# Kernel optimization log

Hardware: AMD Instinct MI355X
Metric: run time of the kernel (lower is better)

The kernel has to match this reference:

```python
import jax, jax.numpy as jnp
import numpy as np

L, D, V, F4 = 12, 768, 50304, 3072
B, T = 4, 1024


def setup_inputs() -> dict:
    key = jax.random.key(0)
    ks = jax.random.split(key, 12)
    s = 0.02
    return {
        "idx": jax.random.randint(ks[0], (B, T), 0, V),
        "targets": jax.random.randint(ks[1], (B, T), 0, V),
        "wte": jax.random.normal(ks[2], (V, D), jnp.float32) * s,  # tied with lm_head
        "pos_embed": jax.random.normal(ks[3], (L, D), jnp.float32),  # per-block (1,1,D) learned pos embed
        "dyt_alpha": jnp.full((L, 3), 0.5, jnp.float32),  # dyt, dyt2, dyt3 alphas
        "dyt_w": jnp.ones((L, 3, D), jnp.float32),
        "dyt_b": jnp.zeros((L, 3, D), jnp.float32),
        "Wq": jax.random.normal(ks[4], (L, D, D), jnp.float32) * s,
        "Wk": jax.random.normal(ks[5], (L, D, D), jnp.float32) * s,
        "Wv": jax.random.normal(ks[6], (L, D, D), jnp.float32) * s,
        "Wp": jax.random.normal(ks[7], (L, D, D), jnp.float32) * s,
        "bp": jnp.zeros((L, D), jnp.float32),
        "We": jax.random.normal(ks[8], (L, F4, D), jnp.float32) * s,
        "be": jnp.zeros((L, F4), jnp.float32),
        "Wc": jax.random.normal(ks[9], (L, D, F4), jnp.float32) * s,
        "bc": jnp.zeros((L, D), jnp.float32),
    }


def _dyt(x, a, w, b):
    return jnp.tanh(a * x) * w + b


def _forward(idx, targets, wte, pos_embed, dyt_alpha, dyt_w, dyt_b,
             Wq, Wk, Wv, Wp, bp, We, be, Wc, bc):
    b, t = idx.shape
    x = wte[idx]  # (b,t,D)
    pos = jnp.arange(t)
    pbias = -jnp.abs(pos[None, :] - pos[:, None]).astype(x.dtype)  # (t,t) ALiBi-style bias
    scale = 1.0 / np.sqrt(D)  # note: source scales by sqrt(emb_dim), not head dim
    total_kl = jnp.asarray(0.0, x.dtype)
    for l in range(L):
        xl = x + pos_embed[l][None, None, :]
        prior = _dyt(xl, dyt_alpha[l, 2], dyt_w[l, 2], dyt_b[l, 2])  # dyt3
        h = _dyt(xl, dyt_alpha[l, 0], dyt_w[l, 0], dyt_b[l, 0])      # dyt (dropout=0)
        Q = jnp.einsum('btd,od->bto', h, Wq[l])
        K = jnp.einsum('btd,od->bto', h, Wk[l])
        Vv = jnp.einsum('btd,od->bto', h, Wv[l])
        scores = jnp.einsum('btd,bsd->bts', Q, K) * scale + pbias  # (b,t,t), no causal mask
        aw = jax.nn.softmax(scores, axis=-1)
        ao = jnp.einsum('bts,bsd->btd', aw, Vv)
        ao = jnp.einsum('btd,od->bto', ao, Wp[l]) + bp[l]
        h2 = _dyt(ao, dyt_alpha[l, 1], dyt_w[l, 1], dyt_b[l, 1])     # dyt2
        h2 = jax.nn.gelu(jnp.einsum('btd,fd->btf', h2, We[l]) + be[l], approximate=False)
        h2 = jnp.einsum('btf,df->btd', h2, Wc[l]) + bc[l]
        posterior = h2 + prior
        m = 0.5 * (prior + posterior)
        lm = jax.nn.log_softmax(m, axis=-1)
        mp = jnp.exp(lm)
        lp = jax.nn.log_softmax(prior, axis=-1)
        lq = jax.nn.log_softmax(posterior, axis=-1)
        # F.kl_div(log_p, q, reduction='batchmean') = sum(q*(log q - log_p)) / batch
        kl = 0.5 * (jnp.sum(mp * (lm - lp)) + jnp.sum(mp * (lm - lq))) / b
        total_kl = total_kl + kl
        x = posterior
    logits = jnp.einsum('btd,vd->btv', x[:, -1:, :], wte)  # (b,1,V)
    full_logits = jnp.einsum('btd,vd->btv', x, wte)
    lsm = jax.nn.log_softmax(full_logits, axis=-1)
    nll = -jnp.take_along_axis(lsm, targets[..., None], axis=-1).squeeze(-1)
    loss = jnp.mean(nll) + total_kl * 0.1
    return logits, loss


def reference(idx, targets, wte, pos_embed, dyt_alpha, dyt_w, dyt_b,
              Wq, Wk, Wv, Wp, bp, We, be, Wc, bc):
    return _forward(idx, targets, wte, pos_embed, dyt_alpha, dyt_w, dyt_b,
                    Wq, Wk, Wv, Wp, bp, We, be, Wc, bc)
```

## Files before the change

kernel.cpp:

```cpp
#include <hip/hip_runtime.h>
#include <hip/hip_bf16.h>

typedef __attribute__((ext_vector_type(8))) short bf16x8;
typedef __attribute__((ext_vector_type(4))) float f32x4;

__device__ __forceinline__ short f2bf(float f) {
  unsigned u = __float_as_uint(f);
  u = u + 0x7fffu + ((u >> 16) & 1u);
  return (short)(u >> 16);
}
__device__ __forceinline__ float bf2f(short s) {
  return __uint_as_float(((unsigned)(unsigned short)s) << 16);
}

#define GLOB_CAST(p) ((const __attribute__((address_space(1))) void*)(p))
#define LDS_CAST(p) ((__attribute__((address_space(3))) void*)(p))
#define GLL16(g, l) __builtin_amdgcn_global_load_lds(GLOB_CAST(g), LDS_CAST(l), 16, 0, 0)

constexpr int EP_BF16 = 0, EP_SCORES = 1, EP_DYT = 2, EP_GELU = 3, EP_PRIOR = 4, EP_QKVT = 5;

__global__ __launch_bounds__(256) void cvt_k(const float* __restrict__ src,
                                             short* __restrict__ dst, long n4) {
  const long s = (long)blockIdx.x * 256 + threadIdx.x;
  if (s >= n4) return;
  float4 v = ((const float4*)src)[s];
  short4 o = {f2bf(v.x), f2bf(v.y), f2bf(v.z), f2bf(v.w)};
  ((short4*)dst)[s] = o;
}

__global__ __launch_bounds__(256) void cvt_layer_k(
    const float* __restrict__ wq, const float* __restrict__ wk,
    const float* __restrict__ wv, const float* __restrict__ wp,
    const float* __restrict__ we, const float* __restrict__ wc,
    short* __restrict__ dst) {
  const long s = (long)blockIdx.x * 256 + threadIdx.x;
  const long e = s * 4;
  const float* src; long off;
  if (e < 589824)        { src = wq; off = e; }
  else if (e < 1179648)  { src = wk; off = e - 589824; }
  else if (e < 1769472)  { src = wv; off = e - 1179648; }
  else if (e < 2359296)  { src = wp; off = e - 1769472; }
  else if (e < 4718592)  { src = we; off = e - 2359296; }
  else                   { src = wc; off = e - 4718592; }
  float4 v = *(const float4*)(src + off);
  short4 o = {f2bf(v.x), f2bf(v.y), f2bf(v.z), f2bf(v.w)};
  *(short4*)(dst + e) = o;
}

__global__ __launch_bounds__(256) void cvt_all_k(
    const float* __restrict__ wq, const float* __restrict__ wk,
    const float* __restrict__ wv, const float* __restrict__ wp,
    const float* __restrict__ we, const float* __restrict__ wc,
    short* __restrict__ dst) {
  const long s = (long)blockIdx.x * 256 + threadIdx.x;
  if (s >= 21233664L) return;
  const long l = s / 1769472;
  const long e = (s - l * 1769472) * 4;
  const float* src; long off;
  if (e < 589824)        { src = wq + l * 589824;  off = e; }
  else if (e < 1179648)  { src = wk + l * 589824;  off = e - 589824; }
  else if (e < 1769472)  { src = wv + l * 589824;  off = e - 1179648; }
  else if (e < 2359296)  { src = wp + l * 589824;  off = e - 1769472; }
  else if (e < 4718592)  { src = we + l * 2359296; off = e - 2359296; }
  else                   { src = wc + l * 2359296; off = e - 4718592; }
  float4 v = *(const float4*)(src + off);
  short4 o = {f2bf(v.x), f2bf(v.y), f2bf(v.z), f2bf(v.w)};
  *(short4*)(dst + l * 7077888 + e) = o;
}

__global__ __launch_bounds__(256) void embed_head_k(
    const int* __restrict__ idx, const float* __restrict__ wte,
    const float* __restrict__ pos, const float* __restrict__ alp,
    const float* __restrict__ w, const float* __restrict__ b,
    float* __restrict__ x, float* __restrict__ prior, short* __restrict__ h) {
  const long s = (long)blockIdx.x * 256 + threadIdx.x;
  const long row = s / 192;
  const int c4 = (int)(s % 192);
  float4 xv = ((const float4*)(wte + (long)idx[row] * 768))[c4];
  ((float4*)x)[s] = xv;
  float4 pv = ((const float4*)pos)[c4];
  float4 w0 = ((const float4*)w)[c4];
  float4 b0 = ((const float4*)b)[c4];
  float4 w2 = ((const float4*)(w + 1536))[c4];
  float4 b2 = ((const float4*)(b + 1536))[c4];
  const float a0 = alp[0], a2 = alp[2];
  float4 xl = {xv.x + pv.x, xv.y + pv.y, xv.z + pv.z, xv.w + pv.w};
  float4 pr = {tanhf(a2 * xl.x) * w2.x + b2.x, tanhf(a2 * xl.y) * w2.y + b2.y,
               tanhf(a2 * xl.z) * w2.z + b2.z, tanhf(a2 * xl.w) * w2.w + b2.w};
  ((float4*)prior)[s] = pr;
  short4 hh = {f2bf(tanhf(a0 * xl.x) * w0.x + b0.x),
               f2bf(tanhf(a0 * xl.y) * w0.y + b0.y),
               f2bf(tanhf(a0 * xl.z) * w0.z + b0.z),
               f2bf(tanhf(a0 * xl.w) * w0.w + b0.w)};
  ((short4*)h)[s] = hh;
}

template <int EP, int TN, int BK>
__global__ __launch_bounds__(256, 2) void gemm_bt(
    const short* __restrict__ A, const short* __restrict__ B,
    void* __restrict__ Cv, short* __restrict__ vt,
    int K, int lda, int ldb, int ldc,
    long sA, long sB, long sC,
    const float* __restrict__ bias, const float* __restrict__ dw,
    const float* __restrict__ db, const float* __restrict__ alp,
    const float* __restrict__ prior, float scale) {
  constexpr int NF = TN / 32;
  constexpr int SEGS = BK / 8;
  constexpr int RPR = 2048 / BK;
  __shared__ short As[128 * BK];
  __shared__ short Bs[TN * BK];
  const int tid = threadIdx.x, lane = tid & 63;
  const int wr = tid >> 7, wc = (tid >> 6) & 1;
  const long rowBase = (long)blockIdx.y * 128;
  const long colBase = (long)blockIdx.x * TN;
  const short* Ab = A + (long)blockIdx.z * sA;
  const short* Bb = B + (long)blockIdx.z * sB;
  const int srow = tid / SEGS, sseg = tid % SEGS;
  const int ssegS = sseg ^ (srow & 7);

  f32x4 acc[4][NF];
#pragma unroll
  for (int m = 0; m < 4; ++m)
#pragma unroll
    for (int n = 0; n < NF; ++n) acc[m][n] = (f32x4){0.f, 0.f, 0.f, 0.f};

  const int q = lane >> 4, cl = lane & 15;
  const int rsw = cl & 7;

  for (int kt = 0; kt < K; kt += BK) {
#pragma unroll
    for (int i = 0; i < BK / 16; ++i) {
      const int row = i * RPR + srow;
      GLL16(Ab + (rowBase + row) * (long)lda + kt + ssegS * 8,
            As + (row * BK + sseg * 8));
    }
#pragma unroll
    for (int i = 0; i < TN * BK / 2048; ++i) {
      const int row = i * RPR + srow;
      GLL16(Bb + (colBase + row) * (long)ldb + kt + ssegS * 8,
            Bs + (row * BK + sseg * 8));
    }
    __syncthreads();
#pragma unroll
    for (int kk = 0; kk < BK / 32; ++kk) {
      const int sw = ((kk * 4 + q) ^ rsw) << 3;
      bf16x8 af[4], bfr[NF];
#pragma unroll
      for (int m = 0; m < 4; ++m)
        af[m] = *(const bf16x8*)&As[(wr * 64 + m * 16 + cl) * BK + sw];
#pragma unroll
      for (int n = 0; n < NF; ++n)
        bfr[n] = *(const bf16x8*)&Bs[(wc * (TN / 2) + n * 16 + cl) * BK + sw];
#pragma unroll
      for (int m = 0; m < 4; ++m)
#pragma unroll
        for (int n = 0; n < NF; ++n)
          acc[m][n] = __builtin_amdgcn_mfma_f32_16x16x32_bf16(af[m], bfr[n], acc[m][n], 0, 0, 0);
    }
    __syncthreads();
  }

#pragma unroll
  for (int m = 0; m < 4; ++m) {
#pragma unroll
    for (int n = 0; n < NF; ++n) {
#pragma unroll
      for (int j = 0; j < 4; ++j) {
        long r = rowBase + wr * 64 + m * 16 + q * 4 + j;
        long c = colBase + wc * (TN / 2) + n * 16 + cl;
        float v = acc[m][n][j];
        if constexpr (EP == EP_SCORES) {
          float pb = -fabsf((float)(int)(r - c));
          ((float*)Cv)[(long)blockIdx.z * sC + r * ldc + c] = v * scale + pb;
        } else if constexpr (EP == EP_BF16) {
          ((short*)Cv)[(long)blockIdx.z * sC + r * ldc + c] = f2bf(v);
        } else if constexpr (EP == EP_QKVT) {
          if (c < 1536)
            ((short*)Cv)[r * (long)ldc + c] = f2bf(v);
          else
            vt[(r >> 10) * 786432 + (c - 1536) * 1024 + (r & 1023)] = f2bf(v);
        } else if constexpr (EP == EP_DYT) {
          float xv = v + bias[c];
          ((short*)Cv)[r * (long)ldc + c] = f2bf(tanhf(alp[0] * xv) * dw[c] + db[c]);
        } else if constexpr (EP == EP_GELU) {
          float xv = v + bias[c];
          ((short*)Cv)[r * (long)ldc + c] = f2bf(0.5f * xv * (1.f + erff(xv * 0.70710678118654752f)));
        } else if constexpr (EP == EP_PRIOR) {
          ((float*)Cv)[r * (long)ldc + c] = v + bias[c] + prior[r * (long)ldc + c];
        }
      }
    }
  }
}

__global__ __launch_bounds__(256) void softmax_k(float* __restrict__ sc) {
  const int lane = threadIdx.x & 63;
  const long row = (long)blockIdx.x * 4 + (threadIdx.x >> 6);
  const float4* p = (const float4*)(sc + row * 1024);
  float4 v[4];
  float mx = -3e38f;
#pragma unroll
  for (int i = 0; i < 4; ++i) {
    v[i] = p[lane * 4 + i];
    mx = fmaxf(mx, fmaxf(fmaxf(v[i].x, v[i].y), fmaxf(v[i].z, v[i].w)));
  }
#pragma unroll
  for (int o = 1; o < 64; o <<= 1) mx = fmaxf(mx, __shfl_xor(mx, o));
  float e[16];
  float s = 0.f;
#pragma unroll
  for (int i = 0; i < 4; ++i) {
    e[i * 4 + 0] = __expf(v[i].x - mx);
    e[i * 4 + 1] = __expf(v[i].y - mx);
    e[i * 4 + 2] = __expf(v[i].z - mx);
    e[i * 4 + 3] = __expf(v[i].w - mx);
    s += e[i * 4] + e[i * 4 + 1] + e[i * 4 + 2] + e[i * 4 + 3];
  }
#pragma unroll
  for (int o = 1; o < 64; o <<= 1) s += __shfl_xor(s, o);
  const float inv = 1.f / s;
  short4* dst = (short4*)((short*)sc + row * 2048);
#pragma unroll
  for (int i = 0; i < 4; ++i) {
    short4 o4 = {f2bf(e[i * 4] * inv), f2bf(e[i * 4 + 1] * inv),
                 f2bf(e[i * 4 + 2] * inv), f2bf(e[i * 4 + 3] * inv)};
    dst[lane * 4 + i] = o4;
  }
}

__global__ __launch_bounds__(256) void tail_k(
    float* __restrict__ prior, const float* __restrict__ post,
    const float* __restrict__ pos_n, const float* __restrict__ alp_n,
    const float* __restrict__ w_n, const float* __restrict__ b_n,
    short* __restrict__ h, short* __restrict__ xbf,
    double* __restrict__ acc, int last) {
  const int lane = threadIdx.x & 63;
  const long row = (long)blockIdx.x * 4 + (threadIdx.x >> 6);
  float* pp = prior + row * 768;
  const float* qq = post + row * 768;
  float p[12], q[12];
#pragma unroll
  for (int i = 0; i < 12; ++i) { p[i] = pp[lane + i * 64]; q[i] = qq[lane + i * 64]; }
  float mp = -3e38f, mq = -3e38f, mm = -3e38f;
#pragma unroll
  for (int i = 0; i < 12; ++i) {
    float m = 0.5f * (p[i] + q[i]);
    mp = fmaxf(mp, p[i]); mq = fmaxf(mq, q[i]); mm = fmaxf(mm, m);
  }
#pragma unroll
  for (int o = 1; o < 64; o <<= 1) {
    mp = fmaxf(mp, __shfl_xor(mp, o));
    mq = fmaxf(mq, __shfl_xor(mq, o));
    mm = fmaxf(mm, __shfl_xor(mm, o));
  }
  float sp = 0.f, sq = 0.f, sm = 0.f;
#pragma unroll
  for (int i = 0; i < 12; ++i) {
    sp += __expf(p[i] - mp);
    sq += __expf(q[i] - mq);
    sm += __expf(0.5f * (p[i] + q[i]) - mm);
  }
#pragma unroll
  for (int o = 1; o < 64; o <<= 1) {
    sp += __shfl_xor(sp, o); sq += __shfl_xor(sq, o); sm += __shfl_xor(sm, o);
  }
  const float lseP = mp + logf(sp), lseQ = mq + logf(sq), lseM = mm + logf(sm);
  float kl = 0.f;
#pragma unroll
  for (int i = 0; i < 12; ++i) {
    float m = 0.5f * (p[i] + q[i]);
    float lm = m - lseM;
    kl += __expf(lm) * (2.f * lm - (p[i] - lseP) - (q[i] - lseQ));
  }
#pragma unroll
  for (int o = 1; o < 64; o <<= 1) kl += __shfl_xor(kl, o);
  if (lane == 0) atomicAdd(&acc[0], (double)kl);

  if (last) {
#pragma unroll
    for (int i = 0; i < 12; ++i) xbf[row * 768 + lane + i * 64] = f2bf(q[i]);
  } else {
    const float a0 = alp_n[0], a2 = alp_n[2];
#pragma unroll
    for (int i = 0; i < 12; ++i) {
      const int col = lane + i * 64;
      float xl = q[i] + pos_n[col];
      pp[col] = tanhf(a2 * xl) * w_n[1536 + col] + b_n[1536 + col];
      h[row * 768 + col] = f2bf(tanhf(a0 * xl) * w_n[col] + b_n[col]);
    }
  }
}

__global__ __launch_bounds__(256, 2) void lse_gemm_k(
    const short* __restrict__ Xb, const short* __restrict__ Wt,
    float* __restrict__ pm, float* __restrict__ ps,
    float* __restrict__ logits_out, int G) {
  __shared__ short As[128 * 64];
  __shared__ short Bs[128 * 64];
  __shared__ float pmx[2][128], psm[2][128], rm[128], rs[128];
  const int tid = threadIdx.x, lane = tid & 63;
  const int wr = tid >> 7, wc = (tid >> 6) & 1;
  const int g = blockIdx.x;
  const long rowBase = (long)blockIdx.y * 128;
  const int srow = tid >> 3, sseg = tid & 7;
  const int ssegS = sseg ^ (srow & 7);
  const int q = lane >> 4, cl = lane & 15;
  const int rsw = cl & 7;
  if (tid < 128) { rm[tid] = -3e38f; rs[tid] = 0.f; }

  for (int tile = g; tile < 393; tile += G) {
    const long colBase = (long)tile * 128;
    f32x4 acc[4][4];
#pragma unroll
    for (int m = 0; m < 4; ++m)
#pragma unroll
      for (int n = 0; n < 4; ++n) acc[m][n] = (f32x4){0.f, 0.f, 0.f, 0.f};

    for (int kt = 0; kt < 768; kt += 64) {
#pragma unroll
      for (int i = 0; i < 4; ++i) {
        GLL16(Xb + (rowBase + i * 32 + srow) * 768L + kt + ssegS * 8,
              As + ((i * 32 + srow) * 64 + sseg * 8));
        GLL16(Wt + (colBase + i * 32 + srow) * 768L + kt + ssegS * 8,
              Bs + ((i * 32 + srow) * 64 + sseg * 8));
      }
      __syncthreads();
#pragma unroll
      for (int kk = 0; kk < 2; ++kk) {
        const int sw = ((kk * 4 + q) ^ rsw) << 3;
        bf16x8 af[4], bfr[4];
#pragma unroll
        for (int m = 0; m < 4; ++m)
          af[m] = *(const bf16x8*)&As[(wr * 64 + m * 16 + cl) * 64 + sw];
#pragma unroll
        for (int n = 0; n < 4; ++n)
          bfr[n] = *(const bf16x8*)&Bs[(wc * 64 + n * 16 + cl) * 64 + sw];
#pragma unroll
        for (int m = 0; m < 4; ++m)
#pragma unroll
          for (int n = 0; n < 4; ++n)
            acc[m][n] = __builtin_amdgcn_mfma_f32_16x16x32_bf16(af[m], bfr[n], acc[m][n], 0, 0, 0);
      }
      __syncthreads();
    }

#pragma unroll
    for (int m = 0; m < 4; ++m)
#pragma unroll
      for (int n = 0; n < 4; ++n)
#pragma unroll
        for (int j = 0; j < 4; ++j) {
          long r = rowBase + wr * 64 + m * 16 + q * 4 + j;
          if ((r & 1023) == 1023) {
            long c = colBase + wc * 64 + n * 16 + cl;
            logits_out[(r >> 10) * 50304 + c] = acc[m][n][j];
          }
        }

#pragma unroll
    for (int m = 0; m < 4; ++m) {
#pragma unroll
      for (int j = 0; j < 4; ++j) {
        float mx = acc[m][0][j];
#pragma unroll
        for (int n = 1; n < 4; ++n) mx = fmaxf(mx, acc[m][n][j]);
#pragma unroll
        for (int o = 1; o < 16; o <<= 1) mx = fmaxf(mx, __shfl_xor(mx, o));
        float sm = 0.f;
#pragma unroll
        for (int n = 0; n < 4; ++n) sm += __expf(acc[m][n][j] - mx);
#pragma unroll
        for (int o = 1; o < 16; o <<= 1) sm += __shfl_xor(sm, o);
        if (cl == 0) {
          int lr = wr * 64 + m * 16 + q * 4 + j;
          pmx[wc][lr] = mx;
          psm[wc][lr] = sm;
        }
      }
    }
    __syncthreads();
    if (tid < 128) {
      float m0 = pmx[0][tid], m1 = pmx[1][tid];
      float m2 = fmaxf(m0, m1);
      float s2 = psm[0][tid] * __expf(m0 - m2) + psm[1][tid] * __expf(m1 - m2);
      float mo = rm[tid], mn = fmaxf(mo, m2);
      rs[tid] = rs[tid] * __expf(mo - mn) + s2 * __expf(m2 - mn);
      rm[tid] = mn;
    }
    __syncthreads();
  }
  if (tid < 128) {
    long row = rowBase + tid;
    pm[row * G + g] = rm[tid];
    ps[row * G + g] = rs[tid];
  }
}

__global__ __launch_bounds__(256) void tlog_k(const short* __restrict__ xbf,
                                              const short* __restrict__ wtebf,
                                              const int* __restrict__ targets,
                                              float* __restrict__ tlog) {
  const int lane = threadIdx.x & 63;
  const long row = (long)blockIdx.x * 4 + (threadIdx.x >> 6);
  const long tgt = targets[row];
  const short* a = xbf + row * 768;
  const short* b = wtebf + tgt * 768;
  float s = 0.f;
#pragma unroll
  for (int i = 0; i < 12; ++i) s += bf2f(a[lane + i * 64]) * bf2f(b[lane + i * 64]);
#pragma unroll
  for (int o = 1; o < 64; o <<= 1) s += __shfl_xor(s, o);
  if (lane == 0) tlog[row] = s;
}

__global__ __launch_bounds__(256) void stage2_k(const float* __restrict__ pm,
                                                const float* __restrict__ ps,
                                                const float* __restrict__ tlog,
                                                double* __restrict__ acc, int G) {
  const long row = (long)blockIdx.x * 256 + threadIdx.x;
  float M = -3e38f;
  for (int gi = 0; gi < G; ++gi) M = fmaxf(M, pm[row * G + gi]);
  float S = 0.f;
  for (int gi = 0; gi < G; ++gi) S += ps[row * G + gi] * __expf(pm[row * G + gi] - M);
  float nll = (M + logf(S)) - tlog[row];
#pragma unroll
  for (int o = 1; o < 64; o <<= 1) nll += __shfl_xor(nll, o);
  if ((threadIdx.x & 63) == 0) atomicAdd(&acc[1], (double)nll);
}

__global__ void finalize_k(const double* __restrict__ acc, float* __restrict__ out) {
  if (threadIdx.x == 0)
    out[201216] = (float)(acc[1] / 4096.0 + 0.1 * 0.5 * acc[0] / 4.0);
}

constexpr size_t OFF_WTEBF = 0;
constexpr size_t OFF_LW    = 77266944;
constexpr size_t OFF_X     = 91422720;
constexpr size_t OFF_PRIOR = 104005632;
constexpr size_t OFF_HB    = 116588544;
constexpr size_t OFF_U1    = 122880000;
constexpr size_t OFF_QKV   = OFF_U1;
constexpr size_t OFF_VT    = OFF_U1 + 18874368;
constexpr size_t OFF_E     = OFF_U1;
constexpr size_t OFF_SC    = 148045824;
constexpr size_t OFF_AO    = 164823040;
constexpr size_t OFF_XBF   = 171114496;
constexpr size_t OFF_PM    = 177405952;
constexpr size_t OFF_PS    = 177799168;
constexpr size_t OFF_TLOG  = 178192384;
constexpr size_t OFF_ACC   = 178208768;
constexpr size_t WS_SMALL  = 178208784;
constexpr size_t OFF_LWALL = 178208784;
constexpr size_t WS_BIG    = 348078096;

extern "C" void kernel_launch(void* const* d_in, const int* in_sizes, int n_in,
                              void* d_out, int out_size, void* d_ws, size_t ws_size,
                              hipStream_t stream) {
  const int* idx = (const int*)d_in[0];
  const int* targets = (const int*)d_in[1];
  const float* wte = (const float*)d_in[2];
  const float* pos = (const float*)d_in[3];
  const float* dalpha = (const float*)d_in[4];
  const float* dytw = (const float*)d_in[5];
  const float* dytb = (const float*)d_in[6];
  const float* Wq = (const float*)d_in[7];
  const float* Wk = (const float*)d_in[8];
  const float* Wv = (const float*)d_in[9];
  const float* Wp = (const float*)d_in[10];
  const float* bp = (const float*)d_in[11];
  const float* We = (const float*)d_in[12];
  const float* be = (const float*)d_in[13];
  const float* Wc = (const float*)d_in[14];
  const float* bc = (const float*)d_in[15];
  float* out = (float*)d_out;

  if (ws_size < WS_SMALL) return;
  const bool big = ws_size >= WS_BIG;
  char* ws = (char*)d_ws;
  short* WTEBF = (short*)(ws + OFF_WTEBF);
  short* LW = (short*)(ws + OFF_LW);
  short* LWALL = (short*)(ws + OFF_LWALL);
  float* X = (float*)(ws + OFF_X);
  float* PRIOR = (float*)(ws + OFF_PRIOR);
  short* HB = (short*)(ws + OFF_HB);
  short* QKVB = (short*)(ws + OFF_QKV);
  short* VT = (short*)(ws + OFF_VT);
  short* E = (short*)(ws + OFF_E);
  float* SC = (float*)(ws + OFF_SC);
  short* AW = (short*)(ws + OFF_SC);
  short* AO = (short*)(ws + OFF_AO);
  short* XBF = (short*)(ws + OFF_XBF);
  float* PM = (float*)(ws + OFF_PM);
  float* PS = (float*)(ws + OFF_PS);
  float* TLOG = (float*)(ws + OFF_TLOG);
  double* ACC = (double*)(ws + OFF_ACC);

  hipMemsetAsync(ACC, 0, 16, stream);
  cvt_k<<<37728, 256, 0, stream>>>(wte, WTEBF, 9658368);
  if (big)
    cvt_all_k<<<82944, 256, 0, stream>>>(Wq, Wk, Wv, Wp, We, Wc, LWALL);
  embed_head_k<<<3072, 256, 0, stream>>>(idx, wte, pos, dalpha, dytw, dytb, X, PRIOR, HB);

  const float scale = 0.03608439182435161f;

  for (int l = 0; l < 12; ++l) {
    const short* lw;
    if (big) {
      lw = LWALL + (long)l * 7077888;
    } else {
      cvt_layer_k<<<6912, 256, 0, stream>>>(Wq + (long)l * 589824, Wk + (long)l * 589824,
                                            Wv + (long)l * 589824, Wp + (long)l * 589824,
                                            We + (long)l * 2359296, Wc + (long)l * 2359296, LW);
      lw = LW;
    }
    gemm_bt<EP_QKVT, 128, 64><<<dim3(18, 32, 1), 256, 0, stream>>>(
        HB, lw, QKVB, VT, 768, 768, 768, 2304, 0, 0, 0,
        nullptr, nullptr, nullptr, nullptr, nullptr, 0.f);
    gemm_bt<EP_SCORES, 64, 128><<<dim3(16, 8, 4), 256, 0, stream>>>(
        QKVB, QKVB + 768, SC, nullptr, 768, 2304, 2304, 1024,
        2359296, 2359296, 1048576, nullptr, nullptr, nullptr, nullptr, nullptr, scale);
    softmax_k<<<1024, 256, 0, stream>>>(SC);
    gemm_bt<EP_BF16, 64, 128><<<dim3(12, 8, 4), 256, 0, stream>>>(
        AW, VT, AO, nullptr, 1024, 2048, 1024, 768, 2097152, 786432, 786432,
        nullptr, nullptr, nullptr, nullptr, nullptr, 0.f);
    gemm_bt<EP_DYT, 64, 128><<<dim3(12, 32, 1), 256, 0, stream>>>(
        AO, lw + 1769472, HB, nullptr, 768, 768, 768, 768, 0, 0, 0,
        bp + l * 768, dytw + l * 2304 + 768, dytb + l * 2304 + 768,
        dalpha + l * 3 + 1, nullptr, 0.f);
    gemm_bt<EP_GELU, 128, 64><<<dim3(24, 32, 1), 256, 0, stream>>>(
        HB, lw + 2359296, E, nullptr, 768, 768, 768, 3072, 0, 0, 0,
        be + l * 3072, nullptr, nullptr, nullptr, nullptr, 0.f);
    gemm_bt<EP_PRIOR, 64, 128><<<dim3(12, 32, 1), 256, 0, stream>>>(
        E, lw + 4718592, X, nullptr, 3072, 3072, 3072, 768, 0, 0, 0,
        bc + l * 768, nullptr, nullptr, nullptr, PRIOR, 0.f);
    tail_k<<<1024, 256, 0, stream>>>(PRIOR, X, pos + (l + 1) * 768,
                                     dalpha + (l + 1) * 3, dytw + (l + 1) * 2304,
                                     dytb + (l + 1) * 2304, HB, XBF, ACC, l == 11);
  }

  lse_gemm_k<<<dim3(24, 32), 256, 0, stream>>>(XBF, WTEBF, PM, PS, out, 24);
  tlog_k<<<1024, 256, 0, stream>>>(XBF, WTEBF, targets, TLOG);
  stage2_k<<<16, 256, 0, stream>>>(PM, PS, TLOG, ACC, 24);
  finalize_k<<<1, 64, 0, stream>>>(ACC, out);
}
```

Measured before the change: 3.280 ms.

## Add TM template tile parameter, shrink small GEMM tiles, use separate V transpose

Makes the GEMM row-tile size a template parameter so the block size scales with it. The scores, attention-output, projection and MLP-down GEMMs now use 64x64 tiles on 128-thread blocks, which gives more blocks on the 256-CU device. The scattered V-transpose store in the QKV epilogue is replaced by a plain bf16 store followed by a separate LDS-tiled transpose kernel. The cost is one extra launch and an extra pass over V per layer, plus lower reuse per tile in the smaller GEMMs.

```diff
diff --git a/kernel.cpp b/kernel.cpp
--- a/kernel.cpp
+++ b/kernel.cpp
@@ -17,7 +17,7 @@
 #define LDS_CAST(p) ((__attribute__((address_space(3))) void*)(p))
 #define GLL16(g, l) __builtin_amdgcn_global_load_lds(GLOB_CAST(g), LDS_CAST(l), 16, 0, 0)
 
-constexpr int EP_BF16 = 0, EP_SCORES = 1, EP_DYT = 2, EP_GELU = 3, EP_PRIOR = 4, EP_QKVT = 5;
+constexpr int EP_BF16 = 0, EP_SCORES = 1, EP_DYT = 2, EP_GELU = 3, EP_PRIOR = 4;
 
 __global__ __launch_bounds__(256) void cvt_k(const float* __restrict__ src,
                                              short* __restrict__ dst, long n4) {
@@ -95,23 +95,24 @@
   ((short4*)h)[s] = hh;
 }
 
-template <int EP, int TN, int BK>
-__global__ __launch_bounds__(256, 2) void gemm_bt(
+template <int EP, int TM, int TN, int BK>
+__global__ __launch_bounds__((TM / 64) * 128, 2) void gemm_bt(
     const short* __restrict__ A, const short* __restrict__ B,
-    void* __restrict__ Cv, short* __restrict__ vt,
-    int K, int lda, int ldb, int ldc,
+    void* __restrict__ Cv, int K, int lda, int ldb, int ldc,
     long sA, long sB, long sC,
     const float* __restrict__ bias, const float* __restrict__ dw,
     const float* __restrict__ db, const float* __restrict__ alp,
     const float* __restrict__ prior, float scale) {
+  constexpr int THREADS = (TM / 64) * 128;
   constexpr int NF = TN / 32;
   constexpr int SEGS = BK / 8;
-  constexpr int RPR = 2048 / BK;
-  __shared__ short As[128 * BK];
+  constexpr int RPR = THREADS / SEGS;
+  __shared__ short As[TM * BK];
   __shared__ short Bs[TN * BK];
   const int tid = threadIdx.x, lane = tid & 63;
-  const int wr = tid >> 7, wc = (tid >> 6) & 1;
-  const long rowBase = (long)blockIdx.y * 128;
+  const int wid = tid >> 6;
+  const int wr = wid >> 1, wc = wid & 1;
+  const long rowBase = (long)blockIdx.y * TM;
   const long colBase = (long)blockIdx.x * TN;
   const short* Ab = A + (long)blockIdx.z * sA;
   const short* Bb = B + (long)blockIdx.z * sB;
@@ -129,13 +130,13 @@
 
   for (int kt = 0; kt < K; kt += BK) {
 #pragma unroll
-    for (int i = 0; i < BK / 16; ++i) {
+    for (int i = 0; i < TM / RPR; ++i) {
       const int row = i * RPR + srow;
       GLL16(Ab + (rowBase + row) * (long)lda + kt + ssegS * 8,
             As + (row * BK + sseg * 8));
     }
 #pragma unroll
-    for (int i = 0; i < TN * BK / 2048; ++i) {
+    for (int i = 0; i < TN / RPR; ++i) {
       const int row = i * RPR + srow;
       GLL16(Bb + (colBase + row) * (long)ldb + kt + ssegS * 8,
             Bs + (row * BK + sseg * 8));
@@ -174,11 +175,6 @@
           ((float*)Cv)[(long)blockIdx.z * sC + r * ldc + c] = v * scale + pb;
         } else if constexpr (EP == EP_BF16) {
           ((short*)Cv)[(long)blockIdx.z * sC + r * ldc + c] = f2bf(v);
-        } else if constexpr (EP == EP_QKVT) {
-          if (c < 1536)
-            ((short*)Cv)[r * (long)ldc + c] = f2bf(v);
-          else
-            vt[(r >> 10) * 786432 + (c - 1536) * 1024 + (r & 1023)] = f2bf(v);
         } else if constexpr (EP == EP_DYT) {
           float xv = v + bias[c];
           ((short*)Cv)[r * (long)ldc + c] = f2bf(tanhf(alp[0] * xv) * dw[c] + db[c]);
@@ -191,6 +187,23 @@
       }
     }
   }
+}
+
+__global__ __launch_bounds__(256) void transp_k(const short* __restrict__ V,
+                                                short* __restrict__ Vt, int ldv) {
+  __shared__ short t[32][33];
+  const int b = blockIdx.z;
+  const int d0 = blockIdx.x * 32, t0 = blockIdx.y * 32;
+  const int tx = threadIdx.x & 31, ty = threadIdx.x >> 5;
+  const short* Vb = V + (long)b * 1024 * ldv;
+  short* Tb = Vt + (long)b * 768 * 1024;
+#pragma unroll
+  for (int i = 0; i < 4; ++i)
+    t[ty + i * 8][tx] = Vb[(long)(t0 + ty + i * 8) * ldv + d0 + tx];
+  __syncthreads();
+#pragma unroll
+  for (int i = 0; i < 4; ++i)
+    Tb[(long)(d0 + ty + i * 8) * 1024 + t0 + tx] = t[tx][ty + i * 8];
 }
 
 __global__ __launch_bounds__(256) void softmax_k(float* __restrict__ sc) {
@@ -513,25 +526,26 @@
                                             We + (long)l * 2359296, Wc + (long)l * 2359296, LW);
       lw = LW;
     }
-    gemm_bt<EP_QKVT, 128, 64><<<dim3(18, 32, 1), 256, 0, stream>>>(
-        HB, lw, QKVB, VT, 768, 768, 768, 2304, 0, 0, 0,
+    gemm_bt<EP_BF16, 128, 128, 64><<<dim3(18, 32, 1), 256, 0, stream>>>(
+        HB, lw, QKVB, 768, 768, 768, 2304, 0, 0, 0,
         nullptr, nullptr, nullptr, nullptr, nullptr, 0.f);
-    gemm_bt<EP_SCORES, 64, 128><<<dim3(16, 8, 4), 256, 0, stream>>>(
-        QKVB, QKVB + 768, SC, nullptr, 768, 2304, 2304, 1024,
+    transp_k<<<dim3(24, 32, 4), 256, 0, stream>>>(QKVB + 1536, VT, 2304);
+    gemm_bt<EP_SCORES, 64, 64, 64><<<dim3(16, 16, 4), 128, 0, stream>>>(
+        QKVB, QKVB + 768, SC, 768, 2304, 2304, 1024,
         2359296, 2359296, 1048576, nullptr, nullptr, nullptr, nullptr, nullptr, scale);
     softmax_k<<<1024, 256, 0, stream>>>(SC);
-    gemm_bt<EP_BF16, 64, 128><<<dim3(12, 8, 4), 256, 0, stream>>>(
-        AW, VT, AO, nullptr, 1024, 2048, 1024, 768, 2097152, 786432, 786432,
+    gemm_bt<EP_BF16, 64, 64, 64><<<dim3(12, 16, 4), 128, 0, stream>>>(
+        AW, VT, AO, 1024, 2048, 1024, 768, 2097152, 786432, 786432,
         nullptr, nullptr, nullptr, nullptr, nullptr, 0.f);
-    gemm_bt<EP_DYT, 64, 128><<<dim3(12, 32, 1), 256, 0, stream>>>(
-        AO, lw + 1769472, HB, nullptr, 768, 768, 768, 768, 0, 0, 0,
+    gemm_bt<EP_DYT, 64, 64, 64><<<dim3(12, 64, 1), 128, 0, stream>>>(
+        AO, lw + 1769472, HB, 768, 768, 768, 768, 0, 0, 0,
         bp + l * 768, dytw + l * 2304 + 768, dytb + l * 2304 + 768,
         dalpha + l * 3 + 1, nullptr, 0.f);
-    gemm_bt<EP_GELU, 128, 64><<<dim3(24, 32, 1), 256, 0, stream>>>(
-        HB, lw + 2359296, E, nullptr, 768, 768, 768, 3072, 0, 0, 0,
+    gemm_bt<EP_GELU, 128, 128, 64><<<dim3(24, 32, 1), 256, 0, stream>>>(
+        HB, lw + 2359296, E, 768, 768, 768, 3072, 0, 0, 0,
         be + l * 3072, nullptr, nullptr, nullptr, nullptr, 0.f);
-    gemm_bt<EP_PRIOR, 64, 128><<<dim3(12, 32, 1), 256, 0, stream>>>(
-        E, lw + 4718592, X, nullptr, 3072, 3072, 3072, 768, 0, 0, 0,
+    gemm_bt<EP_PRIOR, 64, 64, 64><<<dim3(12, 64, 1), 128, 0, stream>>>(
+        E, lw + 4718592, X, 3072, 3072, 3072, 768, 0, 0, 0,
         bc + l * 768, nullptr, nullptr, nullptr, PRIOR, 0.f);
     tail_k<<<1024, 256, 0, stream>>>(PRIOR, X, pos + (l + 1) * 768,
                                      dalpha + (l + 1) * 3, dytw + (l + 1) * 2304,
```

After: 3.265 ms. Within noise of the previous version (-0.5%).
